# Optimization experiments

Measured on AMD Instinct MI355X. Metric: run time of the kernel, lower is better.

Reference implementation:

```python
import jax, jax.numpy as jnp
import numpy as np

C_S = 1024
C_Z = 128
NUM_HEADS = 16
HEAD_DIM = C_S // NUM_HEADS
INF = 1000000.0
LN_EPS = 1e-5


def setup_inputs() -> dict:
    key = jax.random.key(0)
    ks = jax.random.split(key, 12)
    B, N = 2, 768
    s = jax.random.normal(ks[0], (B, N, C_S), dtype=jnp.float32)
    z = jax.random.normal(ks[1], (B, N, N, C_Z), dtype=jnp.float32)
    mask = jnp.ones((B, N), dtype=jnp.float32)
    k_in = jax.random.normal(ks[2], (B, N, C_S), dtype=jnp.float32)
    sc = 1.0 / np.sqrt(C_S)
    Wq = jax.random.normal(ks[3], (C_S, C_S), dtype=jnp.float32) * sc
    bq = jnp.zeros((C_S,), dtype=jnp.float32)
    Wk = jax.random.normal(ks[4], (C_S, C_S), dtype=jnp.float32) * sc
    Wv = jax.random.normal(ks[5], (C_S, C_S), dtype=jnp.float32) * sc
    Wg = jax.random.normal(ks[6], (C_S, C_S), dtype=jnp.float32) * sc
    ln_g = jnp.ones((C_Z,), dtype=jnp.float32)
    ln_b = jnp.zeros((C_Z,), dtype=jnp.float32)
    Wz = jax.random.normal(ks[7], (C_Z, NUM_HEADS), dtype=jnp.float32) / np.sqrt(C_Z)
    # NOTE: module zero-inits proj_o; use small random weights so output/grads are non-trivial.
    Wo = jax.random.normal(ks[8], (C_S, C_S), dtype=jnp.float32) * sc
    return {"s": s, "z": z, "mask": mask, "k_in": k_in,
            "Wq": Wq, "bq": bq, "Wk": Wk, "Wv": Wv, "Wg": Wg,
            "ln_g": ln_g, "ln_b": ln_b, "Wz": Wz, "Wo": Wo}


def reference(s, z, mask, k_in, Wq, bq, Wk, Wv, Wg, ln_g, ln_b, Wz, Wo):
    B, N, _ = s.shape
    H, D = NUM_HEADS, HEAD_DIM
    q = (s @ Wq + bq).reshape(B, N, H, D)
    k = (k_in @ Wk).reshape(B, N, H, D)
    v = (k_in @ Wv).reshape(B, N, H, D)
    # pair bias: LayerNorm(c_z) -> Linear(c_z -> H) -> (B, H, N, N)
    mu = z.mean(axis=-1, keepdims=True)
    var = ((z - mu) ** 2).mean(axis=-1, keepdims=True)
    zn = (z - mu) * jax.lax.rsqrt(var + LN_EPS) * ln_g + ln_b
    bias = jnp.transpose(zn @ Wz, (0, 3, 1, 2))  # (B, H, N, N)
    g = jax.nn.sigmoid(s @ Wg)  # (B, N, C_S)
    attn = jnp.einsum('bihd,bjhd->bhij', q, k) / np.sqrt(D) + bias
    attn = attn + (1.0 - mask)[:, None, None, :] * (-INF)
    p = jax.nn.softmax(attn, axis=-1)
    o = jnp.einsum('bhij,bjhd->bihd', p, v).reshape(B, N, C_S)
    return (g * o) @ Wo
```

## Files before the change

### kernel.cpp

```cpp
#include <hip/hip_runtime.h>
#include <cstdint>


#define B_  2
#define N_  768
#define CS_ 1024
#define CZ_ 128
#define NH_ 16
#define HD_ 64

typedef unsigned short bf16_t;
typedef __attribute__((ext_vector_type(4))) float f32x4;
typedef __attribute__((ext_vector_type(8))) short s16x8;

__device__ __forceinline__ float bflo(uint32_t u){ return __uint_as_float(u<<16); }
__device__ __forceinline__ float bfhi(uint32_t u){ return __uint_as_float(u & 0xFFFF0000u); }
__device__ __forceinline__ float bf2f(bf16_t u){ return __uint_as_float(((uint32_t)u)<<16); }
__device__ __forceinline__ bf16_t f2bf(float f){
  uint32_t x = __float_as_uint(f);
  return (bf16_t)((x + 0x7FFFu + ((x>>16)&1u)) >> 16);
}
__device__ __forceinline__ void unpack8(uint4 q, float* d){
  d[0]=bflo(q.x); d[1]=bfhi(q.x); d[2]=bflo(q.y); d[3]=bfhi(q.y);
  d[4]=bflo(q.z); d[5]=bfhi(q.z); d[6]=bflo(q.w); d[7]=bfhi(q.w);
}
__device__ __forceinline__ void load8f(const void* base, size_t idx, int isbf, float* d){
  if (isbf) { uint4 q = *(const uint4*)((const bf16_t*)base + idx); unpack8(q, d); }
  else {
    const float* p = (const float*)base + idx;
    float4 a = *(const float4*)p, b = *(const float4*)(p+4);
    d[0]=a.x; d[1]=a.y; d[2]=a.z; d[3]=a.w; d[4]=b.x; d[5]=b.y; d[6]=b.z; d[7]=b.w;
  }
}
__device__ __forceinline__ float load1f(const void* base, size_t idx, int isbf){
  return isbf ? bf2f(((const bf16_t*)base)[idx]) : ((const float*)base)[idx];
}
__device__ __forceinline__ void ld16bf(const void* base, size_t idx, int isbf, bf16_t* d){
  if (isbf) {
    const bf16_t* p = (const bf16_t*)base + idx;
    *(uint4*)d = *(const uint4*)p;
    *(uint4*)(d+8) = *(const uint4*)(p+8);
  } else {
    const float* p = (const float*)base + idx;
    #pragma unroll
    for (int e = 0; e < 16; ++e) d[e] = f2bf(p[e]);
  }
}

__global__ void detect_kernel(const uint32_t* __restrict__ mask_bits,
                              const void* __restrict__ Wz,
                              const void* __restrict__ ln_g,
                              const void* __restrict__ ln_b,
                              int* __restrict__ flag, float* __restrict__ AhCh)
{
  const int t = threadIdx.x;
  const int isbf = (mask_bits[0] == 0x3F803F80u) ? 1 : 0;
  if (t == 0) *flag = isbf;
  if (t < 16) {
    float a = 0.0f, c2 = 0.0f;
    for (int c = 0; c < CZ_; ++c) {
      const float w = load1f(Wz, (size_t)c*NH_ + t, isbf);
      a  += load1f(ln_g, c, isbf) * w;
      c2 += load1f(ln_b, c, isbf) * w;
    }
    AhCh[t] = a; AhCh[16 + t] = c2;
  }
}

__global__ __launch_bounds__(256) void prep_wt_kernel(
    const void* __restrict__ Wq, const void* __restrict__ Wk,
    const void* __restrict__ Wv, const void* __restrict__ Wg,
    const void* __restrict__ Wo, bf16_t* __restrict__ WT,
    const int* __restrict__ flagp)
{
  const int isbf = *flagp;
  const int w = blockIdx.z;
  const void* W = (w==0)?Wq:(w==1)?Wk:(w==2)?Wv:(w==3)?Wg:Wo;
  bf16_t* dst = WT + (size_t)w*CS_*CS_;
  __shared__ bf16_t T[64][72];
  const int t = threadIdx.x;
  const int r = t >> 2, c0 = (t & 3) * 16;
  const int k0 = blockIdx.x * 64, n0 = blockIdx.y * 64;
  __align__(16) bf16_t vv[16];
  ld16bf(W, (size_t)(k0 + r)*CS_ + n0 + c0, isbf, vv);
  #pragma unroll
  for (int e = 0; e < 16; ++e) T[r][c0 + e] = vv[e];
  __syncthreads();
  __align__(16) bf16_t ov[16];
  #pragma unroll
  for (int e = 0; e < 16; ++e) ov[e] = T[c0 + e][r];
  bf16_t* op = dst + (size_t)(n0 + r)*CS_ + k0 + c0;
  *(uint4*)op = *(uint4*)&ov[0];
  *(uint4*)(op + 8) = *(uint4*)&ov[8];
}

__global__ __launch_bounds__(256) void pair_bias_kernel(
    const void* __restrict__ z, const void* __restrict__ ln_g,
    const void* __restrict__ Wz, const float* __restrict__ AhCh,
    float* __restrict__ S, const int* __restrict__ flagp)
{
  const int isbf = *flagp;
  __shared__ float Wp[CZ_*NH_];
  const int t = threadIdx.x;
  {
    float wv[8];
    load8f(Wz, (size_t)t*8, isbf, wv);
    const float gc = load1f(ln_g, t >> 1, isbf);
    #pragma unroll
    for (int e = 0; e < 8; ++e) Wp[t*8 + e] = gc * wv[e];
  }
  __syncthreads();

  const int j = blockIdx.x*256 + t, i = blockIdx.y, b = blockIdx.z;
  const size_t zbase = (((size_t)(b*N_ + i))*N_ + j)*CZ_;

  float d[16] = {};
  float s1 = 0.0f, s2 = 0.0f;
  #pragma unroll 2
  for (int cc = 0; cc < CZ_; cc += 8) {
    float zv[8];
    load8f(z, zbase + cc, isbf, zv);
    #pragma unroll
    for (int e = 0; e < 8; ++e) {
      const float zz = zv[e];
      s1 += zz; s2 = fmaf(zz, zz, s2);
      const float4 w0 = *(const float4*)&Wp[(cc+e)*16 + 0];
      const float4 w1 = *(const float4*)&Wp[(cc+e)*16 + 4];
      const float4 w2 = *(const float4*)&Wp[(cc+e)*16 + 8];
      const float4 w3 = *(const float4*)&Wp[(cc+e)*16 + 12];
      d[ 0] = fmaf(zz, w0.x, d[ 0]); d[ 1] = fmaf(zz, w0.y, d[ 1]);
      d[ 2] = fmaf(zz, w0.z, d[ 2]); d[ 3] = fmaf(zz, w0.w, d[ 3]);
      d[ 4] = fmaf(zz, w1.x, d[ 4]); d[ 5] = fmaf(zz, w1.y, d[ 5]);
      d[ 6] = fmaf(zz, w1.z, d[ 6]); d[ 7] = fmaf(zz, w1.w, d[ 7]);
      d[ 8] = fmaf(zz, w2.x, d[ 8]); d[ 9] = fmaf(zz, w2.y, d[ 9]);
      d[10] = fmaf(zz, w2.z, d[10]); d[11] = fmaf(zz, w2.w, d[11]);
      d[12] = fmaf(zz, w3.x, d[12]); d[13] = fmaf(zz, w3.y, d[13]);
      d[14] = fmaf(zz, w3.z, d[14]); d[15] = fmaf(zz, w3.w, d[15]);
    }
  }
  const float mu  = s1 * (1.0f/CZ_);
  const float var = s2 * (1.0f/CZ_) - mu*mu;
  const float rs  = rsqrtf(var + 1e-5f);
  const float am  = -rs * mu;

  float Ah[16], Ch[16];
  #pragma unroll
  for (int p = 0; p < 4; ++p) {
    *(float4*)&Ah[p*4] = *(const float4*)&AhCh[p*4];
    *(float4*)&Ch[p*4] = *(const float4*)&AhCh[16 + p*4];
  }
  const size_t sbase = ((size_t)b*NH_*N_ + i)*N_ + j;
  #pragma unroll
  for (int h = 0; h < 16; ++h) {
    const float bias = fmaf(rs, d[h], fmaf(am, Ah[h], Ch[h]));
    S[sbase + (size_t)h*N_*N_] = bias;
  }
}

__global__ __launch_bounds__(256) void qkvg_mfma_kernel(
    const void* __restrict__ s_in, const void* __restrict__ kin,
    const bf16_t* __restrict__ WT, const void* __restrict__ bq,
    bf16_t* __restrict__ q, bf16_t* __restrict__ k,
    bf16_t* __restrict__ v, float* __restrict__ g,
    const int* __restrict__ flagp)
{
  const int isbf = *flagp;
  __shared__ bf16_t As[128*40];
  __shared__ bf16_t Bs[128*40];
  const int t = threadIdx.x;
  const int bn = blockIdx.x, bm = blockIdx.y;
  const int proj = bn >> 3;
  const void* A = (proj == 0 || proj == 3) ? s_in : kin;
  const bf16_t* WTp = WT + (size_t)proj*CS_*CS_;
  const int n0 = (bn & 7) * 128, m0 = bm * 128;
  const int lane = t & 63, wid = t >> 6;
  const int wr = wid >> 1, wc = wid & 1;
  const int l16 = lane & 15, lq = lane >> 4;
  const int srow = t >> 1, scol = (t & 1) * 16;
  f32x4 acc[4][4] = {};

  for (int k0 = 0; k0 < CS_; k0 += 32) {
    __align__(16) bf16_t av[16];
    ld16bf(A, (size_t)(m0 + srow)*CS_ + k0 + scol, isbf, av);
    {
      const bf16_t* bp = WTp + (size_t)(n0 + srow)*CS_ + k0 + scol;
      *(uint4*)&Bs[srow*40 + scol]     = *(const uint4*)bp;
      *(uint4*)&Bs[srow*40 + scol + 8] = *(const uint4*)(bp + 8);
    }
    *(uint4*)&As[srow*40 + scol]     = *(uint4*)&av[0];
    *(uint4*)&As[srow*40 + scol + 8] = *(uint4*)&av[8];
    __syncthreads();
    s16x8 af[4], bfg[4];
    #pragma unroll
    for (int m = 0; m < 4; ++m)
      af[m] = *(const s16x8*)&As[(wr*64 + m*16 + l16)*40 + lq*8];
    #pragma unroll
    for (int n = 0; n < 4; ++n)
      bfg[n] = *(const s16x8*)&Bs[(wc*64 + n*16 + l16)*40 + lq*8];
    #pragma unroll
    for (int m = 0; m < 4; ++m)
      #pragma unroll
      for (int n = 0; n < 4; ++n)
        acc[m][n] = __builtin_amdgcn_mfma_f32_16x16x32_bf16(af[m], bfg[n], acc[m][n], 0, 0, 0);
    __syncthreads();
  }

  #pragma unroll
  for (int n = 0; n < 4; ++n) {
    const int gc = n0 + wc*64 + n*16 + l16;
    float bqv = 0.0f;
    if (proj == 0) bqv = load1f(bq, gc, isbf);
    #pragma unroll
    for (int m = 0; m < 4; ++m) {
      #pragma unroll
      for (int r = 0; r < 4; ++r) {
        const int gr = m0 + wr*64 + m*16 + lq*4 + r;
        const float val = acc[m][n][r];
        const size_t off = (size_t)gr*CS_ + gc;
        if      (proj == 0) q[off] = f2bf(val + bqv);
        else if (proj == 1) k[off] = f2bf(val);
        else if (proj == 2) v[off] = f2bf(val);
        else                g[off] = 1.0f/(1.0f + __expf(-val));
      }
    }
  }
}

__global__ __launch_bounds__(256) void vt_kernel(
    const bf16_t* __restrict__ v, bf16_t* __restrict__ vt)
{
  __shared__ bf16_t T[64][72];
  const int t = threadIdx.x;
  const int jt = blockIdx.x, bh = blockIdx.y, b = bh >> 4, h = bh & 15;
  const int r = t >> 2, c0 = (t & 3) * 16;
  const int j0 = jt * 64;
  const bf16_t* vp = v + ((size_t)(b*N_ + j0 + r))*CS_ + h*HD_ + c0;
  *(uint4*)&T[r][c0]     = *(const uint4*)vp;
  *(uint4*)&T[r][c0 + 8] = *(const uint4*)(vp + 8);
  __syncthreads();
  __align__(16) bf16_t ov[16];
  #pragma unroll
  for (int e = 0; e < 16; ++e) ov[e] = T[c0 + e][r];
  bf16_t* op = vt + ((size_t)bh*HD_ + r)*N_ + j0 + c0;
  *(uint4*)op       = *(uint4*)&ov[0];
  *(uint4*)(op + 8) = *(uint4*)&ov[8];
}

__global__ __launch_bounds__(256) void attn_s_mfma_kernel(
    const bf16_t* __restrict__ q, const bf16_t* __restrict__ kmat,
    const void* __restrict__ mask, float* __restrict__ S,
    const int* __restrict__ flagp)
{
  const int isbf = *flagp;
  __shared__ bf16_t Qs[128*72];
  __shared__ bf16_t Ks[128*72];
  const int t = threadIdx.x;
  const int mi = blockIdx.x % 6, nj = blockIdx.x / 6;
  const int bh = blockIdx.y, b = bh >> 4, h = bh & 15;
  const int lane = t & 63, wid = t >> 6;
  const int wr = wid >> 1, wc = wid & 1;
  const int l16 = lane & 15, lq = lane >> 4;
  const int srow = t >> 1, scol = (t & 1) * 32;

  {
    const bf16_t* qp = q    + ((size_t)(b*N_ + mi*128 + srow))*CS_ + h*HD_ + scol;
    const bf16_t* kp = kmat + ((size_t)(b*N_ + nj*128 + srow))*CS_ + h*HD_ + scol;
    #pragma unroll
    for (int e = 0; e < 4; ++e) {
      *(uint4*)&Qs[srow*72 + scol + e*8] = *(const uint4*)(qp + e*8);
      *(uint4*)&Ks[srow*72 + scol + e*8] = *(const uint4*)(kp + e*8);
    }
  }
  __syncthreads();
  f32x4 acc[4][4] = {};
  #pragma unroll
  for (int kc = 0; kc < 2; ++kc) {
    s16x8 af[4], bfg[4];
    #pragma unroll
    for (int m = 0; m < 4; ++m)
      af[m] = *(const s16x8*)&Qs[(wr*64 + m*16 + l16)*72 + kc*32 + lq*8];
    #pragma unroll
    for (int n = 0; n < 4; ++n)
      bfg[n] = *(const s16x8*)&Ks[(wc*64 + n*16 + l16)*72 + kc*32 + lq*8];
    #pragma unroll
    for (int m = 0; m < 4; ++m)
      #pragma unroll
      for (int n = 0; n < 4; ++n)
        acc[m][n] = __builtin_amdgcn_mfma_f32_16x16x32_bf16(af[m], bfg[n], acc[m][n], 0, 0, 0);
  }

  const int i0 = mi*128, j0 = nj*128;
  #pragma unroll
  for (int n = 0; n < 4; ++n) {
    const int gj = j0 + wc*64 + n*16 + l16;
    const float mk = load1f(mask, (size_t)b*N_ + gj, isbf);
    const float madd = (1.0f - mk) * (-1.0e6f);
    #pragma unroll
    for (int m = 0; m < 4; ++m) {
      #pragma unroll
      for (int r = 0; r < 4; ++r) {
        const int gi = i0 + wr*64 + m*16 + lq*4 + r;
        float* Sp = S + ((size_t)bh*N_ + gi)*N_ + gj;
        *Sp = fmaf(acc[m][n][r], 0.125f, *Sp) + madd;
      }
    }
  }
}

__global__ __launch_bounds__(256) void softmax_kernel(float* __restrict__ S)
{
  const int t = threadIdx.x, lane = t & 63, w = t >> 6;
  const size_t row = (size_t)blockIdx.x * 4 + w;
  float* Sr = S + row * N_;
  float4 x[3];
  #pragma unroll
  for (int p = 0; p < 3; ++p) x[p] = ((const float4*)Sr)[lane + 64*p];
  float mx = -1.0e30f;
  #pragma unroll
  for (int p = 0; p < 3; ++p)
    mx = fmaxf(mx, fmaxf(fmaxf(x[p].x, x[p].y), fmaxf(x[p].z, x[p].w)));
  #pragma unroll
  for (int m = 1; m <= 32; m <<= 1) mx = fmaxf(mx, __shfl_xor(mx, m));
  float sum = 0.0f;
  #pragma unroll
  for (int p = 0; p < 3; ++p) {
    x[p].x = __expf(x[p].x - mx); x[p].y = __expf(x[p].y - mx);
    x[p].z = __expf(x[p].z - mx); x[p].w = __expf(x[p].w - mx);
    sum += x[p].x + x[p].y + x[p].z + x[p].w;
  }
  #pragma unroll
  for (int m = 1; m <= 32; m <<= 1) sum += __shfl_xor(sum, m);
  const float r = 1.0f / sum;
  #pragma unroll
  for (int p = 0; p < 3; ++p) {
    x[p].x *= r; x[p].y *= r; x[p].z *= r; x[p].w *= r;
    ((float4*)Sr)[lane + 64*p] = x[p];
  }
}

__global__ __launch_bounds__(256) void pv_mfma_kernel(
    const float* __restrict__ S, const bf16_t* __restrict__ vt,
    float* __restrict__ o)
{
  __shared__ bf16_t Ps[64*40];
  __shared__ bf16_t Vs[64*40];
  const int t = threadIdx.x;
  const int mi = blockIdx.x, bh = blockIdx.y, b = bh >> 4, h = bh & 15;
  const int lane = t & 63, wid = t >> 6;
  const int wr = wid >> 1, wc = wid & 1;
  const int l16 = lane & 15, lq = lane >> 4;
  const int srow = t >> 2, scol = (t & 3) * 8;
  const bf16_t* vtb = vt + (size_t)bh*HD_*N_;
  f32x4 acc[2][2] = {};

  for (int k0 = 0; k0 < N_; k0 += 32) {
    {
      const float* Pp = S + ((size_t)bh*N_ + mi*64 + srow)*N_ + k0 + scol;
      float4 f0 = *(const float4*)Pp, f1 = *(const float4*)(Pp + 4);
      __align__(16) bf16_t pv[8];
      pv[0]=f2bf(f0.x); pv[1]=f2bf(f0.y); pv[2]=f2bf(f0.z); pv[3]=f2bf(f0.w);
      pv[4]=f2bf(f1.x); pv[5]=f2bf(f1.y); pv[6]=f2bf(f1.z); pv[7]=f2bf(f1.w);
      *(uint4*)&Ps[srow*40 + scol] = *(uint4*)&pv[0];
    }
    *(uint4*)&Vs[srow*40 + scol] = *(const uint4*)(vtb + (size_t)srow*N_ + k0 + scol);
    __syncthreads();
    s16x8 af[2], bfg[2];
    #pragma unroll
    for (int m = 0; m < 2; ++m)
      af[m] = *(const s16x8*)&Ps[(wr*32 + m*16 + l16)*40 + lq*8];
    #pragma unroll
    for (int n = 0; n < 2; ++n)
      bfg[n] = *(const s16x8*)&Vs[(wc*32 + n*16 + l16)*40 + lq*8];
    #pragma unroll
    for (int m = 0; m < 2; ++m)
      #pragma unroll
      for (int n = 0; n < 2; ++n)
        acc[m][n] = __builtin_amdgcn_mfma_f32_16x16x32_bf16(af[m], bfg[n], acc[m][n], 0, 0, 0);
    __syncthreads();
  }
  #pragma unroll
  for (int m = 0; m < 2; ++m)
    #pragma unroll
    for (int n = 0; n < 2; ++n)
      #pragma unroll
      for (int r = 0; r < 4; ++r) {
        const int gi = mi*64 + wr*32 + m*16 + lq*4 + r;
        const int gd = wc*32 + n*16 + l16;
        o[((size_t)(b*N_ + gi))*CS_ + h*HD_ + gd] = acc[m][n][r];
      }
}

__global__ __launch_bounds__(256) void final_mfma_kernel(
    const float* __restrict__ g, const float* __restrict__ o,
    const bf16_t* __restrict__ WoT, void* __restrict__ out,
    const int* __restrict__ flagp)
{
  const int isbf = *flagp;
  __shared__ bf16_t As[64*40];
  __shared__ bf16_t Bs[64*40];
  const int t = threadIdx.x;
  const int n0 = blockIdx.x * 64, m0 = blockIdx.y * 64;
  const int lane = t & 63, wid = t >> 6;
  const int wr = wid >> 1, wc = wid & 1;
  const int l16 = lane & 15, lq = lane >> 4;
  const int srow = t >> 2, scol = (t & 3) * 8;
  f32x4 acc[2][2] = {};

  for (int k0 = 0; k0 < CS_; k0 += 32) {
    {
      const float* gp = g + (size_t)(m0 + srow)*CS_ + k0 + scol;
      const float* op = o + (size_t)(m0 + srow)*CS_ + k0 + scol;
      float4 g0 = *(const float4*)gp, g1 = *(const float4*)(gp + 4);
      float4 o0 = *(const float4*)op, o1 = *(const float4*)(op + 4);
      __align__(16) bf16_t av[8];
      av[0]=f2bf(g0.x*o0.x); av[1]=f2bf(g0.y*o0.y); av[2]=f2bf(g0.z*o0.z); av[3]=f2bf(g0.w*o0.w);
      av[4]=f2bf(g1.x*o1.x); av[5]=f2bf(g1.y*o1.y); av[6]=f2bf(g1.z*o1.z); av[7]=f2bf(g1.w*o1.w);
      *(uint4*)&As[srow*40 + scol] = *(uint4*)&av[0];
    }
    *(uint4*)&Bs[srow*40 + scol] = *(const uint4*)(WoT + (size_t)(n0 + srow)*CS_ + k0 + scol);
    __syncthreads();
    s16x8 af[2], bfg[2];
    #pragma unroll
    for (int m = 0; m < 2; ++m)
      af[m] = *(const s16x8*)&As[(wr*32 + m*16 + l16)*40 + lq*8];
    #pragma unroll
    for (int n = 0; n < 2; ++n)
      bfg[n] = *(const s16x8*)&Bs[(wc*32 + n*16 + l16)*40 + lq*8];
    #pragma unroll
    for (int m = 0; m < 2; ++m)
      #pragma unroll
      for (int n = 0; n < 2; ++n)
        acc[m][n] = __builtin_amdgcn_mfma_f32_16x16x32_bf16(af[m], bfg[n], acc[m][n], 0, 0, 0);
    __syncthreads();
  }
  #pragma unroll
  for (int m = 0; m < 2; ++m)
    #pragma unroll
    for (int n = 0; n < 2; ++n)
      #pragma unroll
      for (int r = 0; r < 4; ++r) {
        const int gm = m0 + wr*32 + m*16 + lq*4 + r;
        const int gn = n0 + wc*32 + n*16 + l16;
        const float val = acc[m][n][r];
        if (isbf) ((bf16_t*)out)[(size_t)gm*CS_ + gn] = f2bf(val);
        else      ((float*)out)[(size_t)gm*CS_ + gn] = val;
      }
}

extern "C" void kernel_launch(void* const* d_in, const int* in_sizes, int n_in,
                              void* d_out, int out_size, void* d_ws, size_t ws_size,
                              hipStream_t stream)
{
  const void* s_in = d_in[0];
  const void* z    = d_in[1];
  const void* mask = d_in[2];
  const void* k_in = d_in[3];
  const void* Wq   = d_in[4];
  const void* bq   = d_in[5];
  const void* Wk   = d_in[6];
  const void* Wv   = d_in[7];
  const void* Wg   = d_in[8];
  const void* ln_g = d_in[9];
  const void* ln_b = d_in[10];
  const void* Wz   = d_in[11];
  const void* Wo   = d_in[12];

  int*   flag = (int*)d_ws;
  float* AhCh = (float*)d_ws + 16;
  char*  base = (char*)d_ws + 256;

  bf16_t* WT = (bf16_t*)(base);
  bf16_t* q  = (bf16_t*)(base + 10485760);
  bf16_t* k  = (bf16_t*)(base + 13631488);
  bf16_t* v  = (bf16_t*)(base + 16777216);
  bf16_t* vt = (bf16_t*)(base + 19922944);
  float*  g  = (float* )(base + 23068672);
  float*  o  = (float* )(base + 29360128);
  float*  S  = (float* )(base + 35651584);
  bf16_t* WoT = WT + (size_t)4*CS_*CS_;

  detect_kernel<<<1, 64, 0, stream>>>((const uint32_t*)mask, Wz, ln_g, ln_b, flag, AhCh);
  prep_wt_kernel<<<dim3(16, 16, 5), 256, 0, stream>>>(Wq, Wk, Wv, Wg, Wo, WT, flag);
  pair_bias_kernel<<<dim3(3, 768, 2), 256, 0, stream>>>(z, ln_g, Wz, AhCh, S, flag);
  qkvg_mfma_kernel<<<dim3(32, 12), 256, 0, stream>>>(s_in, k_in, WT, bq, q, k, v, g, flag);
  vt_kernel<<<dim3(12, 32), 256, 0, stream>>>(v, vt);
  attn_s_mfma_kernel<<<dim3(36, 32), 256, 0, stream>>>(q, k, mask, S, flag);
  softmax_kernel<<<dim3(6144), 256, 0, stream>>>(S);
  pv_mfma_kernel<<<dim3(12, 32), 256, 0, stream>>>(S, vt, o);
  final_mfma_kernel<<<dim3(16, 24), 256, 0, stream>>>(g, o, WoT, d_out, flag);
}
```

Measured before the change: 1.067 ms.

## Fuse QK scores, softmax and PV into a flash-attention kernel with gated output

Replaces the separate score, softmax and PV kernels with one online-softmax flash kernel. It reads the precomputed pair bias, computes the scores in registers and accumulates P·V without writing the normalized score matrix back. The gating multiply is fused into the epilogue, which writes a bf16 gated output, so the final GEMM loads bf16 directly. This removes several full passes over the B×H×N×N fp32 buffer. In exchange, the grid is small (384 blocks of 64 query rows) and the per-block LDS footprint grows, which can limit parallelism.

```diff
diff --git a/kernel.cpp b/kernel.cpp
--- a/kernel.cpp
+++ b/kernel.cpp
@@ -246,154 +246,147 @@
   *(uint4*)(op + 8) = *(uint4*)&ov[8];
 }
 
-__global__ __launch_bounds__(256) void attn_s_mfma_kernel(
-    const bf16_t* __restrict__ q, const bf16_t* __restrict__ kmat,
-    const void* __restrict__ mask, float* __restrict__ S,
-    const int* __restrict__ flagp)
+#define KPITCH 76
+#define VPITCH 136
+__global__ __launch_bounds__(256) void flash_kernel(
+    const bf16_t* __restrict__ q, const bf16_t* __restrict__ k,
+    const bf16_t* __restrict__ vt, const float* __restrict__ biasS,
+    const void* __restrict__ mask, const float* __restrict__ g,
+    bf16_t* __restrict__ go, const int* __restrict__ flagp)
 {
   const int isbf = *flagp;
-  __shared__ bf16_t Qs[128*72];
-  __shared__ bf16_t Ks[128*72];
-  const int t = threadIdx.x;
-  const int mi = blockIdx.x % 6, nj = blockIdx.x / 6;
-  const int bh = blockIdx.y, b = bh >> 4, h = bh & 15;
-  const int lane = t & 63, wid = t >> 6;
-  const int wr = wid >> 1, wc = wid & 1;
-  const int l16 = lane & 15, lq = lane >> 4;
-  const int srow = t >> 1, scol = (t & 1) * 32;
-
-  {
-    const bf16_t* qp = q    + ((size_t)(b*N_ + mi*128 + srow))*CS_ + h*HD_ + scol;
-    const bf16_t* kp = kmat + ((size_t)(b*N_ + nj*128 + srow))*CS_ + h*HD_ + scol;
-    #pragma unroll
-    for (int e = 0; e < 4; ++e) {
-      *(uint4*)&Qs[srow*72 + scol + e*8] = *(const uint4*)(qp + e*8);
-      *(uint4*)&Ks[srow*72 + scol + e*8] = *(const uint4*)(kp + e*8);
-    }
-  }
-  __syncthreads();
-  f32x4 acc[4][4] = {};
-  #pragma unroll
-  for (int kc = 0; kc < 2; ++kc) {
-    s16x8 af[4], bfg[4];
-    #pragma unroll
-    for (int m = 0; m < 4; ++m)
-      af[m] = *(const s16x8*)&Qs[(wr*64 + m*16 + l16)*72 + kc*32 + lq*8];
-    #pragma unroll
-    for (int n = 0; n < 4; ++n)
-      bfg[n] = *(const s16x8*)&Ks[(wc*64 + n*16 + l16)*72 + kc*32 + lq*8];
-    #pragma unroll
-    for (int m = 0; m < 4; ++m)
-      #pragma unroll
-      for (int n = 0; n < 4; ++n)
-        acc[m][n] = __builtin_amdgcn_mfma_f32_16x16x32_bf16(af[m], bfg[n], acc[m][n], 0, 0, 0);
-  }
-
-  const int i0 = mi*128, j0 = nj*128;
-  #pragma unroll
-  for (int n = 0; n < 4; ++n) {
-    const int gj = j0 + wc*64 + n*16 + l16;
-    const float mk = load1f(mask, (size_t)b*N_ + gj, isbf);
-    const float madd = (1.0f - mk) * (-1.0e6f);
-    #pragma unroll
-    for (int m = 0; m < 4; ++m) {
-      #pragma unroll
-      for (int r = 0; r < 4; ++r) {
-        const int gi = i0 + wr*64 + m*16 + lq*4 + r;
-        float* Sp = S + ((size_t)bh*N_ + gi)*N_ + gj;
-        *Sp = fmaf(acc[m][n][r], 0.125f, *Sp) + madd;
-      }
-    }
-  }
-}
-
-__global__ __launch_bounds__(256) void softmax_kernel(float* __restrict__ S)
-{
-  const int t = threadIdx.x, lane = t & 63, w = t >> 6;
-  const size_t row = (size_t)blockIdx.x * 4 + w;
-  float* Sr = S + row * N_;
-  float4 x[3];
-  #pragma unroll
-  for (int p = 0; p < 3; ++p) x[p] = ((const float4*)Sr)[lane + 64*p];
-  float mx = -1.0e30f;
-  #pragma unroll
-  for (int p = 0; p < 3; ++p)
-    mx = fmaxf(mx, fmaxf(fmaxf(x[p].x, x[p].y), fmaxf(x[p].z, x[p].w)));
-  #pragma unroll
-  for (int m = 1; m <= 32; m <<= 1) mx = fmaxf(mx, __shfl_xor(mx, m));
-  float sum = 0.0f;
-  #pragma unroll
-  for (int p = 0; p < 3; ++p) {
-    x[p].x = __expf(x[p].x - mx); x[p].y = __expf(x[p].y - mx);
-    x[p].z = __expf(x[p].z - mx); x[p].w = __expf(x[p].w - mx);
-    sum += x[p].x + x[p].y + x[p].z + x[p].w;
-  }
-  #pragma unroll
-  for (int m = 1; m <= 32; m <<= 1) sum += __shfl_xor(sum, m);
-  const float r = 1.0f / sum;
-  #pragma unroll
-  for (int p = 0; p < 3; ++p) {
-    x[p].x *= r; x[p].y *= r; x[p].z *= r; x[p].w *= r;
-    ((float4*)Sr)[lane + 64*p] = x[p];
-  }
-}
-
-__global__ __launch_bounds__(256) void pv_mfma_kernel(
-    const float* __restrict__ S, const bf16_t* __restrict__ vt,
-    float* __restrict__ o)
-{
-  __shared__ bf16_t Ps[64*40];
-  __shared__ bf16_t Vs[64*40];
+  __shared__ bf16_t Qs[64*72];
+  __shared__ bf16_t Ks[128*KPITCH];
+  __shared__ bf16_t Vs[64*VPITCH];
+  __shared__ bf16_t Ps[64*VPITCH];
   const int t = threadIdx.x;
   const int mi = blockIdx.x, bh = blockIdx.y, b = bh >> 4, h = bh & 15;
   const int lane = t & 63, wid = t >> 6;
-  const int wr = wid >> 1, wc = wid & 1;
   const int l16 = lane & 15, lq = lane >> 4;
-  const int srow = t >> 2, scol = (t & 3) * 8;
-  const bf16_t* vtb = vt + (size_t)bh*HD_*N_;
-  f32x4 acc[2][2] = {};
-
-  for (int k0 = 0; k0 < N_; k0 += 32) {
+  const int i0 = mi * 64;
+  const int wrow = wid * 16;
+
+  {
+    const int r = t >> 2, c0 = (t & 3) * 16;
+    const bf16_t* qp = q + ((size_t)(b*N_ + i0 + r))*CS_ + h*HD_ + c0;
+    *(uint4*)&Qs[r*72 + c0]     = *(const uint4*)qp;
+    *(uint4*)&Qs[r*72 + c0 + 8] = *(const uint4*)(qp + 8);
+  }
+
+  float m_st[4], l_st[4];
+  #pragma unroll
+  for (int r = 0; r < 4; ++r) { m_st[r] = -1.0e30f; l_st[r] = 0.0f; }
+  f32x4 oacc[4] = {};
+
+  for (int j0 = 0; j0 < N_; j0 += 128) {
     {
-      const float* Pp = S + ((size_t)bh*N_ + mi*64 + srow)*N_ + k0 + scol;
-      float4 f0 = *(const float4*)Pp, f1 = *(const float4*)(Pp + 4);
-      __align__(16) bf16_t pv[8];
-      pv[0]=f2bf(f0.x); pv[1]=f2bf(f0.y); pv[2]=f2bf(f0.z); pv[3]=f2bf(f0.w);
-      pv[4]=f2bf(f1.x); pv[5]=f2bf(f1.y); pv[6]=f2bf(f1.z); pv[7]=f2bf(f1.w);
-      *(uint4*)&Ps[srow*40 + scol] = *(uint4*)&pv[0];
-    }
-    *(uint4*)&Vs[srow*40 + scol] = *(const uint4*)(vtb + (size_t)srow*N_ + k0 + scol);
-    __syncthreads();
-    s16x8 af[2], bfg[2];
-    #pragma unroll
-    for (int m = 0; m < 2; ++m)
-      af[m] = *(const s16x8*)&Ps[(wr*32 + m*16 + l16)*40 + lq*8];
-    #pragma unroll
-    for (int n = 0; n < 2; ++n)
-      bfg[n] = *(const s16x8*)&Vs[(wc*32 + n*16 + l16)*40 + lq*8];
-    #pragma unroll
-    for (int m = 0; m < 2; ++m)
-      #pragma unroll
-      for (int n = 0; n < 2; ++n)
-        acc[m][n] = __builtin_amdgcn_mfma_f32_16x16x32_bf16(af[m], bfg[n], acc[m][n], 0, 0, 0);
-    __syncthreads();
-  }
-  #pragma unroll
-  for (int m = 0; m < 2; ++m)
-    #pragma unroll
-    for (int n = 0; n < 2; ++n)
-      #pragma unroll
-      for (int r = 0; r < 4; ++r) {
-        const int gi = mi*64 + wr*32 + m*16 + lq*4 + r;
-        const int gd = wc*32 + n*16 + l16;
-        o[((size_t)(b*N_ + gi))*CS_ + h*HD_ + gd] = acc[m][n][r];
+      const int r = t >> 1, c0 = (t & 1) * 32;
+      const bf16_t* kp = k + ((size_t)(b*N_ + j0 + r))*CS_ + h*HD_ + c0;
+      #pragma unroll
+      for (int e = 0; e < 4; ++e)
+        *(uint4*)&Ks[r*KPITCH + c0 + e*8] = *(const uint4*)(kp + e*8);
+      const int vr = t >> 2, vc = (t & 3) * 32;
+      const bf16_t* vp = vt + ((size_t)bh*HD_ + vr)*N_ + j0 + vc;
+      #pragma unroll
+      for (int e = 0; e < 4; ++e)
+        *(uint4*)&Vs[vr*VPITCH + vc + e*8] = *(const uint4*)(vp + e*8);
+    }
+    __syncthreads();
+
+    f32x4 sacc[8] = {};
+    #pragma unroll
+    for (int kc = 0; kc < 2; ++kc) {
+      const s16x8 af = *(const s16x8*)&Qs[(wrow + l16)*72 + kc*32 + lq*8];
+      s16x8 bfg[8];
+      #pragma unroll
+      for (int n = 0; n < 8; ++n)
+        bfg[n] = *(const s16x8*)&Ks[(n*16 + l16)*KPITCH + kc*32 + lq*8];
+      #pragma unroll
+      for (int n = 0; n < 8; ++n)
+        sacc[n] = __builtin_amdgcn_mfma_f32_16x16x32_bf16(af, bfg[n], sacc[n], 0, 0, 0);
+    }
+
+    float madd[8];
+    #pragma unroll
+    for (int n = 0; n < 8; ++n) {
+      const int gj = j0 + n*16 + l16;
+      madd[n] = (1.0f - load1f(mask, (size_t)b*N_ + gj, isbf)) * (-1.0e6f);
+    }
+    float pvv[8][4];
+    float scl[4];
+    #pragma unroll
+    for (int r = 0; r < 4; ++r) {
+      const int gi = i0 + wrow + lq*4 + r;
+      const float* bp = biasS + ((size_t)bh*N_ + gi)*N_ + j0;
+      float tmax = -1.0e30f;
+      #pragma unroll
+      for (int n = 0; n < 8; ++n) {
+        const float sv = fmaf(sacc[n][r], 0.125f, bp[n*16 + l16]) + madd[n];
+        pvv[n][r] = sv;
+        tmax = fmaxf(tmax, sv);
       }
+      #pragma unroll
+      for (int msk = 1; msk <= 8; msk <<= 1)
+        tmax = fmaxf(tmax, __shfl_xor(tmax, msk));
+      const float newm = fmaxf(m_st[r], tmax);
+      scl[r] = __expf(m_st[r] - newm);
+      float rsum = 0.0f;
+      #pragma unroll
+      for (int n = 0; n < 8; ++n) {
+        const float p = __expf(pvv[n][r] - newm);
+        pvv[n][r] = p;
+        rsum += p;
+      }
+      #pragma unroll
+      for (int msk = 1; msk <= 8; msk <<= 1)
+        rsum += __shfl_xor(rsum, msk);
+      l_st[r] = l_st[r] * scl[r] + rsum;
+      m_st[r] = newm;
+    }
+    #pragma unroll
+    for (int n = 0; n < 4; ++n)
+      #pragma unroll
+      for (int r = 0; r < 4; ++r)
+        oacc[n][r] *= scl[r];
+
+    #pragma unroll
+    for (int n = 0; n < 8; ++n)
+      #pragma unroll
+      for (int r = 0; r < 4; ++r)
+        Ps[(wrow + lq*4 + r)*VPITCH + n*16 + l16] = f2bf(pvv[n][r]);
+    __syncthreads();
+
+    #pragma unroll
+    for (int kc = 0; kc < 4; ++kc) {
+      const s16x8 af = *(const s16x8*)&Ps[(wrow + l16)*VPITCH + kc*32 + lq*8];
+      s16x8 bfg[4];
+      #pragma unroll
+      for (int n = 0; n < 4; ++n)
+        bfg[n] = *(const s16x8*)&Vs[(n*16 + l16)*VPITCH + kc*32 + lq*8];
+      #pragma unroll
+      for (int n = 0; n < 4; ++n)
+        oacc[n] = __builtin_amdgcn_mfma_f32_16x16x32_bf16(af, bfg[n], oacc[n], 0, 0, 0);
+    }
+    __syncthreads();
+  }
+
+  #pragma unroll
+  for (int r = 0; r < 4; ++r) {
+    const float rl = 1.0f / l_st[r];
+    const int gi = i0 + wrow + lq*4 + r;
+    #pragma unroll
+    for (int n = 0; n < 4; ++n) {
+      const int gd = h*HD_ + n*16 + l16;
+      const size_t off = ((size_t)(b*N_ + gi))*CS_ + gd;
+      const float val = oacc[n][r] * rl;
+      go[off] = f2bf(g[off] * val);
+    }
+  }
 }
 
 __global__ __launch_bounds__(256) void final_mfma_kernel(
-    const float* __restrict__ g, const float* __restrict__ o,
-    const bf16_t* __restrict__ WoT, void* __restrict__ out,
-    const int* __restrict__ flagp)
+    const bf16_t* __restrict__ go, const bf16_t* __restrict__ WoT,
+    void* __restrict__ out, const int* __restrict__ flagp)
 {
   const int isbf = *flagp;
   __shared__ bf16_t As[64*40];
@@ -407,16 +400,7 @@
   f32x4 acc[2][2] = {};
 
   for (int k0 = 0; k0 < CS_; k0 += 32) {
-    {
-      const float* gp = g + (size_t)(m0 + srow)*CS_ + k0 + scol;
-      const float* op = o + (size_t)(m0 + srow)*CS_ + k0 + scol;
-      float4 g0 = *(const float4*)gp, g1 = *(const float4*)(gp + 4);
-      float4 o0 = *(const float4*)op, o1 = *(const float4*)(op + 4);
-      __align__(16) bf16_t av[8];
-      av[0]=f2bf(g0.x*o0.x); av[1]=f2bf(g0.y*o0.y); av[2]=f2bf(g0.z*o0.z); av[3]=f2bf(g0.w*o0.w);
-      av[4]=f2bf(g1.x*o1.x); av[5]=f2bf(g1.y*o1.y); av[6]=f2bf(g1.z*o1.z); av[7]=f2bf(g1.w*o1.w);
-      *(uint4*)&As[srow*40 + scol] = *(uint4*)&av[0];
-    }
+    *(uint4*)&As[srow*40 + scol] = *(const uint4*)(go  + (size_t)(m0 + srow)*CS_ + k0 + scol);
     *(uint4*)&Bs[srow*40 + scol] = *(const uint4*)(WoT + (size_t)(n0 + srow)*CS_ + k0 + scol);
     __syncthreads();
     s16x8 af[2], bfg[2];
@@ -474,9 +458,9 @@
   bf16_t* k  = (bf16_t*)(base + 13631488);
   bf16_t* v  = (bf16_t*)(base + 16777216);
   bf16_t* vt = (bf16_t*)(base + 19922944);
-  float*  g  = (float* )(base + 23068672);
-  float*  o  = (float* )(base + 29360128);
-  float*  S  = (float* )(base + 35651584);
+  bf16_t* go = (bf16_t*)(base + 23068672);
+  float*  g  = (float* )(base + 26214400);
+  float*  S  = (float* )(base + 32505856);
   bf16_t* WoT = WT + (size_t)4*CS_*CS_;
 
   detect_kernel<<<1, 64, 0, stream>>>((const uint32_t*)mask, Wz, ln_g, ln_b, flag, AhCh);
@@ -484,8 +468,6 @@
   pair_bias_kernel<<<dim3(3, 768, 2), 256, 0, stream>>>(z, ln_g, Wz, AhCh, S, flag);
   qkvg_mfma_kernel<<<dim3(32, 12), 256, 0, stream>>>(s_in, k_in, WT, bq, q, k, v, g, flag);
   vt_kernel<<<dim3(12, 32), 256, 0, stream>>>(v, vt);
-  attn_s_mfma_kernel<<<dim3(36, 32), 256, 0, stream>>>(q, k, mask, S, flag);
-  softmax_kernel<<<dim3(6144), 256, 0, stream>>>(S);
-  pv_mfma_kernel<<<dim3(12, 32), 256, 0, stream>>>(S, vt, o);
-  final_mfma_kernel<<<dim3(16, 24), 256, 0, stream>>>(g, o, WoT, d_out, flag);
-}
+  flash_kernel<<<dim3(12, 32), 256, 0, stream>>>(q, k, vt, S, mask, g, go, flag);
+  final_mfma_kernel<<<dim3(16, 24), 256, 0, stream>>>(go, WoT, d_out, flag);
+}
```

Measured after the change: 1.014 ms. 1.05x faster.
